# Kernel tuning notes

Measured on AMD Instinct MI355X. Metric: run time of the kernel, lower is better.

Reference implementation:

```python
import jax, jax.numpy as jnp
import numpy as np

N_NODES = 50000
VOCAB = 2048
HID = 256
N_EDGES = 1600000


def setup_inputs() -> dict:
    key = jax.random.key(0)
    ks = jax.random.split(key, 7)
    context = jax.random.normal(ks[0], (N_NODES, VOCAB), dtype=jnp.float32)
    adj_row = jax.random.randint(ks[1], (N_EDGES,), 0, N_NODES, dtype=jnp.int64)
    adj_col = jax.random.randint(ks[2], (N_EDGES,), 0, N_NODES, dtype=jnp.int64)
    adj_val = jax.random.uniform(ks[3], (N_EDGES,), dtype=jnp.float32)
    # learned params
    context_weight = jax.random.normal(ks[4], (HID, VOCAB), dtype=jnp.float32) * 0.02
    out_w = jax.random.normal(ks[5], (VOCAB, HID), dtype=jnp.float32) * 0.02
    out_b = jnp.zeros((VOCAB,), dtype=jnp.float32)
    return {
        "context": context,
        "adj_row": adj_row,
        "adj_col": adj_col,
        "adj_val": adj_val,
        "context_weight": context_weight,
        "out_w": out_w,
        "out_b": out_b,
    }


def reference(context, adj_row, adj_col, adj_val, context_weight, out_w, out_b):
    # support = context @ context_weight.T : [N, hid]
    support = jnp.einsum('nv,hv->nh', context, context_weight)
    # spmm: out[r] += val * support[c]  (COO sparse-dense matmul)
    gathered = support[adj_col] * adj_val[:, None]          # [E, hid]
    agg = jax.ops.segment_sum(gathered, adj_row, num_segments=N_NODES)  # [N, hid]
    score = jax.nn.relu(agg)
    # out linear: hid -> vocab
    output = jnp.einsum('nh,vh->nv', score, out_w) + out_b  # [N, vocab]
    return output
```

## Files before the change

kernel.cpp:

```cpp
#include <hip/hip_runtime.h>
#include <hip/hip_bf16.h>

#define N_NODES 50000
#define VOCAB   2048
#define HID     256
#define N_EDGES 1600000

typedef __attribute__((ext_vector_type(8))) __bf16 bf16x8;
typedef __attribute__((ext_vector_type(4))) __bf16 bf16x4;
typedef __attribute__((ext_vector_type(4))) float  f32x4;

__device__ __forceinline__ void gl_lds16(const void* g, void* l) {
    __builtin_amdgcn_global_load_lds(
        (const __attribute__((address_space(1))) void*)g,
        (__attribute__((address_space(3))) void*)l, 16, 0, 0);
}

#define ZERO_NB 49
__global__ __launch_bounds__(256) void phase1(
    const float* __restrict__ w, __bf16* __restrict__ wb, int n4,
    int* __restrict__ cnt, int ncnt)
{
    int bid = blockIdx.x;
    if (bid < ZERO_NB) {
        const int base = bid * 1024 + threadIdx.x * 4;
        if (base + 3 < ncnt)      *(int4*)&cnt[base] = make_int4(0, 0, 0, 0);
        else                      for (int i = 0; i < 4; ++i)
                                      if (base + i < ncnt) cnt[base + i] = 0;
        return;
    }
    const int t = (bid - ZERO_NB) * 256 + threadIdx.x;
    if (t < n4) {
        const float4 v = ((const float4*)w)[t];
        bf16x4 p = { (__bf16)v.x, (__bf16)v.y, (__bf16)v.z, (__bf16)v.w };
        ((bf16x4*)wb)[t] = p;
    }
}

#define HIST_NB 96
#define CVTW_NB 64
__global__ __launch_bounds__(256) void phase2(
    const float*  __restrict__ Af,
    const __bf16* __restrict__ Bb,
    __bf16*       __restrict__ Cb,
    int M,
    const int*    __restrict__ arow, int* __restrict__ cnt, int E,
    const float*  __restrict__ w2,   __bf16* __restrict__ w2b, int n4w)
{
    const int tid = threadIdx.x;
    int bid = blockIdx.x;

    if (bid < HIST_NB) {
        const int stride = HIST_NB * 256;
        for (int e4 = bid * 256 + tid; e4 < E / 4; e4 += stride) {
            const int4 r = ((const int4*)arow)[e4];
            atomicAdd(&cnt[r.x], 1); atomicAdd(&cnt[r.y], 1);
            atomicAdd(&cnt[r.z], 1); atomicAdd(&cnt[r.w], 1);
        }
        return;
    }
    bid -= HIST_NB;
    if (bid < CVTW_NB) {
        const int stride = CVTW_NB * 256;
        for (int t = bid * 256 + tid; t < n4w; t += stride) {
            const float4 v = ((const float4*)w2)[t];
            bf16x4 p = { (__bf16)v.x, (__bf16)v.y, (__bf16)v.z, (__bf16)v.w };
            ((bf16x4*)w2b)[t] = p;
        }
        return;
    }
    bid -= CVTW_NB;

    constexpr int K = 2048, N = 256, BM = 64, BK = 32, nkt = K / BK;
    __shared__ float  sAf[3][BM * BK];
    __shared__ __bf16 sB [3][N  * BK];

    const int lane = tid & 63;
    const int wn   = tid >> 6;
    const int half = lane >> 4;
    const int r16  = lane & 15;
    const int m0   = bid * BM;

    f32x4 acc[4][4] = {};

    auto stage = [&](int kt, int b) {
        const int k0 = kt * BK;
        #pragma unroll
        for (int i = 0; i < 2; ++i) {
            const int s   = i * 256 + tid;
            const int row = s >> 3, c = s & 7;
            const int csw = c ^ (row & 7);
            int gr = m0 + row; if (gr >= M) gr = M - 1;
            gl_lds16(&Af[(size_t)gr * K + k0 + csw * 4], &sAf[b][s * 4]);
        }
        #pragma unroll
        for (int i = 0; i < 4; ++i) {
            const int s   = i * 256 + tid;
            const int row = s >> 2, c = s & 3;
            const int csw = c ^ (row & 3);
            gl_lds16(&Bb[(size_t)row * K + k0 + csw * 8], &sB[b][s * 8]);
        }
    };
    auto step = [&](int b) {
        bf16x8 bfr[4];
        #pragma unroll
        for (int n = 0; n < 4; ++n) {
            const int brow = wn * 64 + n * 16 + r16;
            bfr[n] = *(const bf16x8*)&sB[b][brow * 32 + (half ^ (brow & 3)) * 8];
        }
        #pragma unroll
        for (int m = 0; m < 4; ++m) {
            const int arw = m * 16 + r16;
            const int rx  = arw & 7;
            const f32x4 lo = *(const f32x4*)&sAf[b][arw * 32 + ((2 * half)     ^ rx) * 4];
            const f32x4 hi = *(const f32x4*)&sAf[b][arw * 32 + ((2 * half + 1) ^ rx) * 4];
            const bf16x8 af = { (__bf16)lo.x, (__bf16)lo.y, (__bf16)lo.z, (__bf16)lo.w,
                                (__bf16)hi.x, (__bf16)hi.y, (__bf16)hi.z, (__bf16)hi.w };
            #pragma unroll
            for (int n = 0; n < 4; ++n)
                acc[m][n] = __builtin_amdgcn_mfma_f32_16x16x32_bf16(
                                af, bfr[n], acc[m][n], 0, 0, 0);
        }
    };

    stage(0, 0);
    stage(1, 1);
    for (int t = 0; t < nkt; ++t) {
        if (t + 1 < nkt) asm volatile("s_waitcnt vmcnt(6)" ::: "memory");
        else             asm volatile("s_waitcnt vmcnt(0)" ::: "memory");
        __builtin_amdgcn_s_barrier();
        __builtin_amdgcn_sched_barrier(0);
        step(t % 3);
        if (t + 2 < nkt) stage(t + 2, (t + 2) % 3);
    }

    #pragma unroll
    for (int m = 0; m < 4; ++m) {
        #pragma unroll
        for (int j = 0; j < 4; ++j) {
            const int gr = m0 + m * 16 + half * 4 + j;
            if (gr >= M) continue;
            #pragma unroll
            for (int n = 0; n < 4; ++n) {
                const int gc = wn * 64 + n * 16 + r16;
                Cb[(size_t)gr * N + gc] = (__bf16)acc[m][n][j];
            }
        }
    }
}

#define SCAN_NB 49

__global__ __launch_bounds__(256) void scan1(
    const int* __restrict__ cnt, int* __restrict__ bsum, int n)
{
    __shared__ int red[256];
    const int base = blockIdx.x * 1024 + threadIdx.x * 4;
    int s = 0;
    #pragma unroll
    for (int i = 0; i < 4; ++i) { const int idx = base + i; if (idx < n) s += cnt[idx]; }
    red[threadIdx.x] = s;
    __syncthreads();
    for (int off = 128; off > 0; off >>= 1) {
        if (threadIdx.x < off) red[threadIdx.x] += red[threadIdx.x + off];
        __syncthreads();
    }
    if (threadIdx.x == 0) bsum[blockIdx.x] = red[0];
}

__global__ __launch_bounds__(64) void scan2(int* __restrict__ bsum, int nb)
{
    if (threadIdx.x == 0) {
        int run = 0;
        for (int b = 0; b < nb; ++b) { const int v = bsum[b]; bsum[b] = run; run += v; }
        bsum[nb] = run;
    }
}

__global__ __launch_bounds__(256) void scan3(
    const int* __restrict__ cnt, const int* __restrict__ bsum,
    int* __restrict__ ptr, int* __restrict__ cursor, int n)
{
    __shared__ int hs[256];
    const int base = blockIdx.x * 1024 + threadIdx.x * 4;
    int loc[4]; int s = 0;
    #pragma unroll
    for (int i = 0; i < 4; ++i) {
        const int idx = base + i;
        loc[i] = (idx < n) ? cnt[idx] : 0;
        s += loc[i];
    }
    hs[threadIdx.x] = s;
    __syncthreads();
    for (int off = 1; off < 256; off <<= 1) {
        int v = (threadIdx.x >= off) ? hs[threadIdx.x - off] : 0;
        __syncthreads();
        hs[threadIdx.x] += v;
        __syncthreads();
    }
    int run = bsum[blockIdx.x] + ((threadIdx.x == 0) ? 0 : hs[threadIdx.x - 1]);
    #pragma unroll
    for (int i = 0; i < 4; ++i) {
        const int idx = base + i;
        if (idx < n) { ptr[idx] = run; cursor[idx] = run; }
        run += loc[i];
    }
    if (blockIdx.x == SCAN_NB - 1 && threadIdx.x == 255) ptr[n] = run;
}

__global__ __launch_bounds__(256) void csr_fill(
    const int*   __restrict__ arow,
    const int*   __restrict__ acol,
    const float* __restrict__ aval,
    int*         __restrict__ cursor,
    int2*        __restrict__ cpair,
    int E)
{
    const int stride = gridDim.x * blockDim.x;
    for (int e4 = blockIdx.x * blockDim.x + threadIdx.x; e4 < E / 4; e4 += stride) {
        const int4   r = ((const int4*)arow)[e4];
        const int4   c = ((const int4*)acol)[e4];
        const float4 v = ((const float4*)aval)[e4];
        int p;
        p = atomicAdd(&cursor[r.x], 1); cpair[p] = make_int2(c.x, __float_as_int(v.x));
        p = atomicAdd(&cursor[r.y], 1); cpair[p] = make_int2(c.y, __float_as_int(v.y));
        p = atomicAdd(&cursor[r.z], 1); cpair[p] = make_int2(c.z, __float_as_int(v.z));
        p = atomicAdd(&cursor[r.w], 1); cpair[p] = make_int2(c.w, __float_as_int(v.w));
    }
}

__global__ __launch_bounds__(256) void spmm_gather(
    const int*    __restrict__ ptr,
    const int2*   __restrict__ cpair,
    const __bf16* __restrict__ support,
    __bf16*       __restrict__ agg,
    int n)
{
    const int tid  = threadIdx.x;
    const int lane = tid & 63;
    const int row  = blockIdx.x * 4 + (tid >> 6);
    if (row >= n) return;
    const int l32 = lane & 31, ep = lane >> 5;
    const int beg = ptr[row], end = ptr[row + 1];

    float a[8] = {0.f, 0.f, 0.f, 0.f, 0.f, 0.f, 0.f, 0.f};

    auto fma8 = [&](float v, const uint4& s) {
        a[0] += v * __uint_as_float(s.x << 16);
        a[1] += v * __uint_as_float(s.x & 0xFFFF0000u);
        a[2] += v * __uint_as_float(s.y << 16);
        a[3] += v * __uint_as_float(s.y & 0xFFFF0000u);
        a[4] += v * __uint_as_float(s.z << 16);
        a[5] += v * __uint_as_float(s.z & 0xFFFF0000u);
        a[6] += v * __uint_as_float(s.w << 16);
        a[7] += v * __uint_as_float(s.w & 0xFFFF0000u);
    };

    int i = beg;
    for (; i + 8 <= end; i += 8) {
        const int2 p0 = cpair[i + ep];
        const int2 p1 = cpair[i + 2 + ep];
        const int2 p2 = cpair[i + 4 + ep];
        const int2 p3 = cpair[i + 6 + ep];
        const uint4 s0 = *(const uint4*)&support[(size_t)p0.x * HID + l32 * 8];
        const uint4 s1 = *(const uint4*)&support[(size_t)p1.x * HID + l32 * 8];
        const uint4 s2 = *(const uint4*)&support[(size_t)p2.x * HID + l32 * 8];
        const uint4 s3 = *(const uint4*)&support[(size_t)p3.x * HID + l32 * 8];
        fma8(__int_as_float(p0.y), s0);
        fma8(__int_as_float(p1.y), s1);
        fma8(__int_as_float(p2.y), s2);
        fma8(__int_as_float(p3.y), s3);
    }
    for (; i + 2 <= end; i += 2) {
        const int2 p = cpair[i + ep];
        const uint4 s = *(const uint4*)&support[(size_t)p.x * HID + l32 * 8];
        fma8(__int_as_float(p.y), s);
    }
    if (i < end && ep == 0) {
        const int2 p = cpair[i];
        const uint4 s = *(const uint4*)&support[(size_t)p.x * HID + l32 * 8];
        fma8(__int_as_float(p.y), s);
    }

    #pragma unroll
    for (int k = 0; k < 8; ++k) a[k] += __shfl_xor(a[k], 32);

    if (ep == 0) {
        bf16x8 o = { (__bf16)fmaxf(a[0], 0.f), (__bf16)fmaxf(a[1], 0.f),
                     (__bf16)fmaxf(a[2], 0.f), (__bf16)fmaxf(a[3], 0.f),
                     (__bf16)fmaxf(a[4], 0.f), (__bf16)fmaxf(a[5], 0.f),
                     (__bf16)fmaxf(a[6], 0.f), (__bf16)fmaxf(a[7], 0.f) };
        *(bf16x8*)&agg[(size_t)row * HID + l32 * 8] = o;
    }
}

__global__ __launch_bounds__(256) void gemm2(
    const __bf16* __restrict__ Ab,
    const __bf16* __restrict__ Bb,
    const float*  __restrict__ bias,
    float*        __restrict__ C,
    int M)
{
    constexpr int K = 256, N = 2048, BM = 128, BN = 128, BK = 32;
    constexpr int NBY = N / BN, nkt = K / BK;
    __shared__ __bf16 sA[3][BM * BK];
    __shared__ __bf16 sB[3][BN * BK];

    const int tid  = threadIdx.x;
    const int lane = tid & 63;
    const int wid  = tid >> 6;
    const int wm   = wid >> 1;
    const int wn   = wid & 1;
    const int half = lane >> 4;
    const int r16  = lane & 15;

    const int nwg = gridDim.x, cpx = nwg >> 3;
    const int wg  = (blockIdx.x & 7) * cpx + (blockIdx.x >> 3);
    const int m0  = (wg / NBY) * BM;
    const int n0  = (wg % NBY) * BN;

    f32x4 acc[4][4] = {};

    auto stage = [&](int kt, int b) {
        const int k0 = kt * BK;
        #pragma unroll
        for (int i = 0; i < 2; ++i) {
            const int s   = i * 256 + tid;
            const int row = s >> 2, c = s & 3;
            const int csw = c ^ (row & 3);
            int gr = m0 + row; if (gr >= M) gr = M - 1;
            gl_lds16(&Ab[(size_t)gr * K + k0 + csw * 8], &sA[b][s * 8]);
        }
        #pragma unroll
        for (int i = 0; i < 2; ++i) {
            const int s   = i * 256 + tid;
            const int row = s >> 2, c = s & 3;
            const int csw = c ^ (row & 3);
            gl_lds16(&Bb[(size_t)(n0 + row) * K + k0 + csw * 8], &sB[b][s * 8]);
        }
    };
    auto step = [&](int b) {
        bf16x8 bfr[4];
        #pragma unroll
        for (int n = 0; n < 4; ++n) {
            const int brow = wn * 64 + n * 16 + r16;
            bfr[n] = *(const bf16x8*)&sB[b][brow * 32 + (half ^ (brow & 3)) * 8];
        }
        #pragma unroll
        for (int m = 0; m < 4; ++m) {
            const int arw = wm * 64 + m * 16 + r16;
            const bf16x8 af = *(const bf16x8*)&sA[b][arw * 32 + (half ^ (arw & 3)) * 8];
            #pragma unroll
            for (int n = 0; n < 4; ++n)
                acc[m][n] = __builtin_amdgcn_mfma_f32_16x16x32_bf16(
                                af, bfr[n], acc[m][n], 0, 0, 0);
        }
    };

    stage(0, 0);
    stage(1, 1);
    for (int t = 0; t < nkt; ++t) {
        if (t + 1 < nkt) asm volatile("s_waitcnt vmcnt(4)" ::: "memory");
        else             asm volatile("s_waitcnt vmcnt(0)" ::: "memory");
        __builtin_amdgcn_s_barrier();
        __builtin_amdgcn_sched_barrier(0);
        step(t % 3);
        if (t + 2 < nkt) stage(t + 2, (t + 2) % 3);
    }

    #pragma unroll
    for (int m = 0; m < 4; ++m) {
        #pragma unroll
        for (int j = 0; j < 4; ++j) {
            const int gr = m0 + wm * 64 + m * 16 + half * 4 + j;
            if (gr >= M) continue;
            #pragma unroll
            for (int n = 0; n < 4; ++n) {
                const int gc = n0 + wn * 64 + n * 16 + r16;
                __builtin_nontemporal_store(acc[m][n][j] + bias[gc],
                                            &C[(size_t)gr * N + gc]);
            }
        }
    }
}

extern "C" void kernel_launch(void* const* d_in, const int* in_sizes, int n_in,
                              void* d_out, int out_size, void* d_ws, size_t ws_size,
                              hipStream_t stream) {
    const float* context  = (const float*)d_in[0];
    const int*   adj_row  = (const int*)  d_in[1];
    const int*   adj_col  = (const int*)  d_in[2];
    const float* adj_val  = (const float*)d_in[3];
    const float* ctx_w    = (const float*)d_in[4];
    const float* out_w    = (const float*)d_in[5];
    const float* out_b    = (const float*)d_in[6];
    float*       out      = (float*)d_out;

    char* ws = (char*)d_ws;
    __bf16* support_b = (__bf16*)ws;  ws += (size_t)N_NODES * HID * 2;
    __bf16* agg_b     = (__bf16*)ws;  ws += (size_t)N_NODES * HID * 2;
    __bf16* ctxw_b    = (__bf16*)ws;  ws += (size_t)HID * VOCAB * 2;
    __bf16* outw_b    = (__bf16*)ws;  ws += (size_t)VOCAB * HID * 2;
    int*    csr_ptr   = (int*)ws;     ws += ((size_t)N_NODES + 16) * 4;
    int*    cnt       = (int*)ws;     ws += (size_t)N_NODES * 4;
    int*    cursor    = (int*)ws;     ws += (size_t)N_NODES * 4;
    int*    bsum      = (int*)ws;     ws += ((size_t)SCAN_NB + 16) * 4;
    int2*   cpair     = (int2*)ws;    ws += (size_t)N_EDGES * 8;

    constexpr int N4 = HID * VOCAB / 4;

    phase1<<<dim3(ZERO_NB + (N4 + 255) / 256), 256, 0, stream>>>(
        ctx_w, ctxw_b, N4, cnt, N_NODES);

    phase2<<<dim3(HIST_NB + CVTW_NB + (N_NODES + 63) / 64), 256, 0, stream>>>(
        context, ctxw_b, support_b, N_NODES,
        adj_row, cnt, N_EDGES,
        out_w, outw_b, N4);

    scan1<<<SCAN_NB, 256, 0, stream>>>(cnt, bsum, N_NODES);
    scan2<<<1, 64, 0, stream>>>(bsum, SCAN_NB);
    scan3<<<SCAN_NB, 256, 0, stream>>>(cnt, bsum, csr_ptr, cursor, N_NODES);

    csr_fill<<<512, 256, 0, stream>>>(
        adj_row, adj_col, adj_val, cursor, cpair, N_EDGES);

    spmm_gather<<<(N_NODES + 3) / 4, 256, 0, stream>>>(
        csr_ptr, cpair, support_b, agg_b, N_NODES);

    gemm2<<<dim3(((N_NODES + 127) / 128) * (VOCAB / 128)), 256, 0, stream>>>(
        agg_b, outw_b, out_b, out, N_NODES);
}
```

Before: 491.9 us.

## Regroup launches: fuse CSR fill with first GEMM, load B operand directly

Moves the context GEMM out of the histogram kernel and into the CSR fill kernel, so the fill's atomic scatter overlaps the dense matmul. Histogram and both weight conversions now share one launch, and a memset zeroes the counts. Both GEMMs stop staging the weight operand in LDS and read B fragments straight from global memory, with A double-buffered and synced by __syncthreads. This cuts LDS traffic and frees capacity, but exposes global latency on B loads and replaces the hand-tuned vmcnt pipeline with full barriers.

```diff
diff --git a/kernel.cpp b/kernel.cpp
--- a/kernel.cpp
+++ b/kernel.cpp
@@ -16,40 +16,15 @@
         (__attribute__((address_space(3))) void*)l, 16, 0, 0);
 }
 
-#define ZERO_NB 49
+#define HIST_NB 256
+#define CVT_NB  512
 __global__ __launch_bounds__(256) void phase1(
-    const float* __restrict__ w, __bf16* __restrict__ wb, int n4,
-    int* __restrict__ cnt, int ncnt)
-{
-    int bid = blockIdx.x;
-    if (bid < ZERO_NB) {
-        const int base = bid * 1024 + threadIdx.x * 4;
-        if (base + 3 < ncnt)      *(int4*)&cnt[base] = make_int4(0, 0, 0, 0);
-        else                      for (int i = 0; i < 4; ++i)
-                                      if (base + i < ncnt) cnt[base + i] = 0;
-        return;
-    }
-    const int t = (bid - ZERO_NB) * 256 + threadIdx.x;
-    if (t < n4) {
-        const float4 v = ((const float4*)w)[t];
-        bf16x4 p = { (__bf16)v.x, (__bf16)v.y, (__bf16)v.z, (__bf16)v.w };
-        ((bf16x4*)wb)[t] = p;
-    }
-}
-
-#define HIST_NB 96
-#define CVTW_NB 64
-__global__ __launch_bounds__(256) void phase2(
-    const float*  __restrict__ Af,
-    const __bf16* __restrict__ Bb,
-    __bf16*       __restrict__ Cb,
-    int M,
-    const int*    __restrict__ arow, int* __restrict__ cnt, int E,
-    const float*  __restrict__ w2,   __bf16* __restrict__ w2b, int n4w)
+    const int*   __restrict__ arow, int* __restrict__ cnt, int E,
+    const float* __restrict__ w1, __bf16* __restrict__ w1b,
+    const float* __restrict__ w2, __bf16* __restrict__ w2b)
 {
     const int tid = threadIdx.x;
     int bid = blockIdx.x;
-
     if (bid < HIST_NB) {
         const int stride = HIST_NB * 256;
         for (int e4 = bid * 256 + tid; e4 < E / 4; e4 += stride) {
@@ -60,20 +35,108 @@
         return;
     }
     bid -= HIST_NB;
-    if (bid < CVTW_NB) {
-        const int stride = CVTW_NB * 256;
-        for (int t = bid * 256 + tid; t < n4w; t += stride) {
-            const float4 v = ((const float4*)w2)[t];
-            bf16x4 p = { (__bf16)v.x, (__bf16)v.y, (__bf16)v.z, (__bf16)v.w };
-            ((bf16x4*)w2b)[t] = p;
+    const float* w  = (bid < CVT_NB) ? w1 : w2;
+    __bf16*      wb = (bid < CVT_NB) ? w1b : w2b;
+    if (bid >= CVT_NB) bid -= CVT_NB;
+    const int t = bid * 256 + tid;
+    const float4 v = ((const float4*)w)[t];
+    bf16x4 p = { (__bf16)v.x, (__bf16)v.y, (__bf16)v.z, (__bf16)v.w };
+    ((bf16x4*)wb)[t] = p;
+}
+
+#define SCAN_NB 49
+
+__global__ __launch_bounds__(256) void scan1(
+    const int* __restrict__ cnt, int* __restrict__ bsum, int n)
+{
+    __shared__ int red[256];
+    const int base = blockIdx.x * 1024 + threadIdx.x * 4;
+    int s = 0;
+    #pragma unroll
+    for (int i = 0; i < 4; ++i) { const int idx = base + i; if (idx < n) s += cnt[idx]; }
+    red[threadIdx.x] = s;
+    __syncthreads();
+    for (int off = 128; off > 0; off >>= 1) {
+        if (threadIdx.x < off) red[threadIdx.x] += red[threadIdx.x + off];
+        __syncthreads();
+    }
+    if (threadIdx.x == 0) bsum[blockIdx.x] = red[0];
+}
+
+__global__ __launch_bounds__(64) void scan2(int* __restrict__ bsum, int nb)
+{
+    if (threadIdx.x == 0) {
+        int run = 0;
+        for (int b = 0; b < nb; ++b) { const int v = bsum[b]; bsum[b] = run; run += v; }
+        bsum[nb] = run;
+    }
+}
+
+__global__ __launch_bounds__(256) void scan3(
+    const int* __restrict__ cnt, const int* __restrict__ bsum,
+    int* __restrict__ ptr, int* __restrict__ cursor, int n)
+{
+    __shared__ int hs[256];
+    const int base = blockIdx.x * 1024 + threadIdx.x * 4;
+    int loc[4]; int s = 0;
+    #pragma unroll
+    for (int i = 0; i < 4; ++i) {
+        const int idx = base + i;
+        loc[i] = (idx < n) ? cnt[idx] : 0;
+        s += loc[i];
+    }
+    hs[threadIdx.x] = s;
+    __syncthreads();
+    for (int off = 1; off < 256; off <<= 1) {
+        int v = (threadIdx.x >= off) ? hs[threadIdx.x - off] : 0;
+        __syncthreads();
+        hs[threadIdx.x] += v;
+        __syncthreads();
+    }
+    int run = bsum[blockIdx.x] + ((threadIdx.x == 0) ? 0 : hs[threadIdx.x - 1]);
+    #pragma unroll
+    for (int i = 0; i < 4; ++i) {
+        const int idx = base + i;
+        if (idx < n) { ptr[idx] = run; cursor[idx] = run; }
+        run += loc[i];
+    }
+    if (blockIdx.x == SCAN_NB - 1 && threadIdx.x == 255) ptr[n] = run;
+}
+
+#define FILL_NB 256
+__global__ __launch_bounds__(256) void fill_gemm1(
+    const int*    __restrict__ arow,
+    const int*    __restrict__ acol,
+    const float*  __restrict__ aval,
+    int*          __restrict__ cursor,
+    int2*         __restrict__ cpair,
+    int E,
+    const float*  __restrict__ Af,
+    const __bf16* __restrict__ Bb,
+    __bf16*       __restrict__ Cb,
+    int M)
+{
+    const int tid = threadIdx.x;
+    int bid = blockIdx.x;
+
+    if (bid < FILL_NB) {
+        const int stride = FILL_NB * 256;
+        for (int e4 = bid * 256 + tid; e4 < E / 4; e4 += stride) {
+            const int4   r = ((const int4*)arow)[e4];
+            const int4   c = ((const int4*)acol)[e4];
+            const float4 v = ((const float4*)aval)[e4];
+            int p;
+            p = atomicAdd(&cursor[r.x], 1); cpair[p] = make_int2(c.x, __float_as_int(v.x));
+            p = atomicAdd(&cursor[r.y], 1); cpair[p] = make_int2(c.y, __float_as_int(v.y));
+            p = atomicAdd(&cursor[r.z], 1); cpair[p] = make_int2(c.z, __float_as_int(v.z));
+            p = atomicAdd(&cursor[r.w], 1); cpair[p] = make_int2(c.w, __float_as_int(v.w));
         }
         return;
     }
-    bid -= CVTW_NB;
+    bid -= FILL_NB;
 
     constexpr int K = 2048, N = 256, BM = 64, BK = 32, nkt = K / BK;
-    __shared__ float  sAf[3][BM * BK];
-    __shared__ __bf16 sB [3][N  * BK];
+    __shared__ float sAf[2][BM * BK];
 
     const int lane = tid & 63;
     const int wn   = tid >> 6;
@@ -83,7 +146,7 @@
 
     f32x4 acc[4][4] = {};
 
-    auto stage = [&](int kt, int b) {
+    auto stageA = [&](int kt, int b) {
         const int k0 = kt * BK;
         #pragma unroll
         for (int i = 0; i < 2; ++i) {
@@ -93,21 +156,19 @@
             int gr = m0 + row; if (gr >= M) gr = M - 1;
             gl_lds16(&Af[(size_t)gr * K + k0 + csw * 4], &sAf[b][s * 4]);
         }
-        #pragma unroll
-        for (int i = 0; i < 4; ++i) {
-            const int s   = i * 256 + tid;
-            const int row = s >> 2, c = s & 3;
-            const int csw = c ^ (row & 3);
-            gl_lds16(&Bb[(size_t)row * K + k0 + csw * 8], &sB[b][s * 8]);
-        }
     };
-    auto step = [&](int b) {
-        bf16x8 bfr[4];
+
+    stageA(0, 0);
+    __syncthreads();
+    for (int t = 0; t < nkt; ++t) {
+        uint4 bq[4];
         #pragma unroll
         for (int n = 0; n < 4; ++n) {
             const int brow = wn * 64 + n * 16 + r16;
-            bfr[n] = *(const bf16x8*)&sB[b][brow * 32 + (half ^ (brow & 3)) * 8];
-        }
+            bq[n] = *(const uint4*)&Bb[(size_t)brow * K + t * BK + half * 8];
+        }
+        if (t + 1 < nkt) stageA(t + 1, (t + 1) & 1);
+        const int b = t & 1;
         #pragma unroll
         for (int m = 0; m < 4; ++m) {
             const int arw = m * 16 + r16;
@@ -119,19 +180,9 @@
             #pragma unroll
             for (int n = 0; n < 4; ++n)
                 acc[m][n] = __builtin_amdgcn_mfma_f32_16x16x32_bf16(
-                                af, bfr[n], acc[m][n], 0, 0, 0);
-        }
-    };
-
-    stage(0, 0);
-    stage(1, 1);
-    for (int t = 0; t < nkt; ++t) {
-        if (t + 1 < nkt) asm volatile("s_waitcnt vmcnt(6)" ::: "memory");
-        else             asm volatile("s_waitcnt vmcnt(0)" ::: "memory");
-        __builtin_amdgcn_s_barrier();
-        __builtin_amdgcn_sched_barrier(0);
-        step(t % 3);
-        if (t + 2 < nkt) stage(t + 2, (t + 2) % 3);
+                                af, *(const bf16x8*)&bq[n], acc[m][n], 0, 0, 0);
+        }
+        __syncthreads();
     }
 
     #pragma unroll
@@ -146,86 +197,6 @@
                 Cb[(size_t)gr * N + gc] = (__bf16)acc[m][n][j];
             }
         }
-    }
-}
-
-#define SCAN_NB 49
-
-__global__ __launch_bounds__(256) void scan1(
-    const int* __restrict__ cnt, int* __restrict__ bsum, int n)
-{
-    __shared__ int red[256];
-    const int base = blockIdx.x * 1024 + threadIdx.x * 4;
-    int s = 0;
-    #pragma unroll
-    for (int i = 0; i < 4; ++i) { const int idx = base + i; if (idx < n) s += cnt[idx]; }
-    red[threadIdx.x] = s;
-    __syncthreads();
-    for (int off = 128; off > 0; off >>= 1) {
-        if (threadIdx.x < off) red[threadIdx.x] += red[threadIdx.x + off];
-        __syncthreads();
-    }
-    if (threadIdx.x == 0) bsum[blockIdx.x] = red[0];
-}
-
-__global__ __launch_bounds__(64) void scan2(int* __restrict__ bsum, int nb)
-{
-    if (threadIdx.x == 0) {
-        int run = 0;
-        for (int b = 0; b < nb; ++b) { const int v = bsum[b]; bsum[b] = run; run += v; }
-        bsum[nb] = run;
-    }
-}
-
-__global__ __launch_bounds__(256) void scan3(
-    const int* __restrict__ cnt, const int* __restrict__ bsum,
-    int* __restrict__ ptr, int* __restrict__ cursor, int n)
-{
-    __shared__ int hs[256];
-    const int base = blockIdx.x * 1024 + threadIdx.x * 4;
-    int loc[4]; int s = 0;
-    #pragma unroll
-    for (int i = 0; i < 4; ++i) {
-        const int idx = base + i;
-        loc[i] = (idx < n) ? cnt[idx] : 0;
-        s += loc[i];
-    }
-    hs[threadIdx.x] = s;
-    __syncthreads();
-    for (int off = 1; off < 256; off <<= 1) {
-        int v = (threadIdx.x >= off) ? hs[threadIdx.x - off] : 0;
-        __syncthreads();
-        hs[threadIdx.x] += v;
-        __syncthreads();
-    }
-    int run = bsum[blockIdx.x] + ((threadIdx.x == 0) ? 0 : hs[threadIdx.x - 1]);
-    #pragma unroll
-    for (int i = 0; i < 4; ++i) {
-        const int idx = base + i;
-        if (idx < n) { ptr[idx] = run; cursor[idx] = run; }
-        run += loc[i];
-    }
-    if (blockIdx.x == SCAN_NB - 1 && threadIdx.x == 255) ptr[n] = run;
-}
-
-__global__ __launch_bounds__(256) void csr_fill(
-    const int*   __restrict__ arow,
-    const int*   __restrict__ acol,
-    const float* __restrict__ aval,
-    int*         __restrict__ cursor,
-    int2*        __restrict__ cpair,
-    int E)
-{
-    const int stride = gridDim.x * blockDim.x;
-    for (int e4 = blockIdx.x * blockDim.x + threadIdx.x; e4 < E / 4; e4 += stride) {
-        const int4   r = ((const int4*)arow)[e4];
-        const int4   c = ((const int4*)acol)[e4];
-        const float4 v = ((const float4*)aval)[e4];
-        int p;
-        p = atomicAdd(&cursor[r.x], 1); cpair[p] = make_int2(c.x, __float_as_int(v.x));
-        p = atomicAdd(&cursor[r.y], 1); cpair[p] = make_int2(c.y, __float_as_int(v.y));
-        p = atomicAdd(&cursor[r.z], 1); cpair[p] = make_int2(c.z, __float_as_int(v.z));
-        p = atomicAdd(&cursor[r.w], 1); cpair[p] = make_int2(c.w, __float_as_int(v.w));
     }
 }
 
@@ -303,8 +274,7 @@
 {
     constexpr int K = 256, N = 2048, BM = 128, BN = 128, BK = 32;
     constexpr int NBY = N / BN, nkt = K / BK;
-    __shared__ __bf16 sA[3][BM * BK];
-    __shared__ __bf16 sB[3][BN * BK];
+    __shared__ __bf16 sA[2][BM * BK];
 
     const int tid  = threadIdx.x;
     const int lane = tid & 63;
@@ -321,7 +291,7 @@
 
     f32x4 acc[4][4] = {};
 
-    auto stage = [&](int kt, int b) {
+    auto stageA = [&](int kt, int b) {
         const int k0 = kt * BK;
         #pragma unroll
         for (int i = 0; i < 2; ++i) {
@@ -331,21 +301,19 @@
             int gr = m0 + row; if (gr >= M) gr = M - 1;
             gl_lds16(&Ab[(size_t)gr * K + k0 + csw * 8], &sA[b][s * 8]);
         }
-        #pragma unroll
-        for (int i = 0; i < 2; ++i) {
-            const int s   = i * 256 + tid;
-            const int row = s >> 2, c = s & 3;
-            const int csw = c ^ (row & 3);
-            gl_lds16(&Bb[(size_t)(n0 + row) * K + k0 + csw * 8], &sB[b][s * 8]);
-        }
     };
-    auto step = [&](int b) {
-        bf16x8 bfr[4];
+
+    stageA(0, 0);
+    __syncthreads();
+    for (int t = 0; t < nkt; ++t) {
+        uint4 bq[4];
         #pragma unroll
         for (int n = 0; n < 4; ++n) {
-            const int brow = wn * 64 + n * 16 + r16;
-            bfr[n] = *(const bf16x8*)&sB[b][brow * 32 + (half ^ (brow & 3)) * 8];
-        }
+            const int brow = n0 + wn * 64 + n * 16 + r16;
+            bq[n] = *(const uint4*)&Bb[(size_t)brow * K + t * BK + half * 8];
+        }
+        if (t + 1 < nkt) stageA(t + 1, (t + 1) & 1);
+        const int b = t & 1;
         #pragma unroll
         for (int m = 0; m < 4; ++m) {
             const int arw = wm * 64 + m * 16 + r16;
@@ -353,19 +321,9 @@
             #pragma unroll
             for (int n = 0; n < 4; ++n)
                 acc[m][n] = __builtin_amdgcn_mfma_f32_16x16x32_bf16(
-                                af, bfr[n], acc[m][n], 0, 0, 0);
-        }
-    };
-
-    stage(0, 0);
-    stage(1, 1);
-    for (int t = 0; t < nkt; ++t) {
-        if (t + 1 < nkt) asm volatile("s_waitcnt vmcnt(4)" ::: "memory");
-        else             asm volatile("s_waitcnt vmcnt(0)" ::: "memory");
-        __builtin_amdgcn_s_barrier();
-        __builtin_amdgcn_sched_barrier(0);
-        step(t % 3);
-        if (t + 2 < nkt) stage(t + 2, (t + 2) % 3);
+                                af, *(const bf16x8*)&bq[n], acc[m][n], 0, 0, 0);
+        }
+        __syncthreads();
     }
 
     #pragma unroll
@@ -407,22 +365,18 @@
     int*    bsum      = (int*)ws;     ws += ((size_t)SCAN_NB + 16) * 4;
     int2*   cpair     = (int2*)ws;    ws += (size_t)N_EDGES * 8;
 
-    constexpr int N4 = HID * VOCAB / 4;
-
-    phase1<<<dim3(ZERO_NB + (N4 + 255) / 256), 256, 0, stream>>>(
-        ctx_w, ctxw_b, N4, cnt, N_NODES);
-
-    phase2<<<dim3(HIST_NB + CVTW_NB + (N_NODES + 63) / 64), 256, 0, stream>>>(
-        context, ctxw_b, support_b, N_NODES,
-        adj_row, cnt, N_EDGES,
-        out_w, outw_b, N4);
+    hipMemsetAsync(cnt, 0, (size_t)N_NODES * 4, stream);
+
+    phase1<<<dim3(HIST_NB + 2 * CVT_NB), 256, 0, stream>>>(
+        adj_row, cnt, N_EDGES, ctx_w, ctxw_b, out_w, outw_b);
 
     scan1<<<SCAN_NB, 256, 0, stream>>>(cnt, bsum, N_NODES);
     scan2<<<1, 64, 0, stream>>>(bsum, SCAN_NB);
     scan3<<<SCAN_NB, 256, 0, stream>>>(cnt, bsum, csr_ptr, cursor, N_NODES);
 
-    csr_fill<<<512, 256, 0, stream>>>(
-        adj_row, adj_col, adj_val, cursor, cpair, N_EDGES);
+    fill_gemm1<<<dim3(FILL_NB + (N_NODES + 63) / 64), 256, 0, stream>>>(
+        adj_row, adj_col, adj_val, cursor, cpair, N_EDGES,
+        context, ctxw_b, support_b, N_NODES);
 
     spmm_gather<<<(N_NODES + 3) / 4, 256, 0, stream>>>(
         csr_ptr, cpair, support_b, agg_b, N_NODES);
```

New measurement: 581.9 us. 18.3% more time.

## Fuse block-prefix scan into final scan kernel and deepen SpMM gather unroll

Applied to the files above, without the earlier changes.

Removes the single-threaded scan2 kernel. Each scan3m block now reduces the preceding block sums itself in shared memory, which saves one kernel launch and a serial pass. The final pointer is set directly to the edge count. Separately, the SpMM gather loop now handles 16 edges per iteration with 8 independent support loads in flight to raise memory-level parallelism, at the cost of more registers and a longer remainder path for short rows.

```diff
diff --git a/kernel.cpp b/kernel.cpp
--- a/kernel.cpp
+++ b/kernel.cpp
@@ -168,21 +168,22 @@
     if (threadIdx.x == 0) bsum[blockIdx.x] = red[0];
 }
 
-__global__ __launch_bounds__(64) void scan2(int* __restrict__ bsum, int nb)
-{
-    if (threadIdx.x == 0) {
-        int run = 0;
-        for (int b = 0; b < nb; ++b) { const int v = bsum[b]; bsum[b] = run; run += v; }
-        bsum[nb] = run;
-    }
-}
-
-__global__ __launch_bounds__(256) void scan3(
+__global__ __launch_bounds__(256) void scan3m(
     const int* __restrict__ cnt, const int* __restrict__ bsum,
-    int* __restrict__ ptr, int* __restrict__ cursor, int n)
+    int* __restrict__ ptr, int* __restrict__ cursor, int n, int E)
 {
     __shared__ int hs[256];
-    const int base = blockIdx.x * 1024 + threadIdx.x * 4;
+    __shared__ int pre[256];
+    const int tid = threadIdx.x;
+    pre[tid] = (tid < blockIdx.x && tid < SCAN_NB) ? bsum[tid] : 0;
+    __syncthreads();
+    for (int off = 128; off > 0; off >>= 1) {
+        if (tid < off) pre[tid] += pre[tid + off];
+        __syncthreads();
+    }
+    const int bbase = pre[0];
+
+    const int base = blockIdx.x * 1024 + tid * 4;
     int loc[4]; int s = 0;
     #pragma unroll
     for (int i = 0; i < 4; ++i) {
@@ -190,22 +191,22 @@
         loc[i] = (idx < n) ? cnt[idx] : 0;
         s += loc[i];
     }
-    hs[threadIdx.x] = s;
+    hs[tid] = s;
     __syncthreads();
     for (int off = 1; off < 256; off <<= 1) {
-        int v = (threadIdx.x >= off) ? hs[threadIdx.x - off] : 0;
+        int v = (tid >= off) ? hs[tid - off] : 0;
         __syncthreads();
-        hs[threadIdx.x] += v;
+        hs[tid] += v;
         __syncthreads();
     }
-    int run = bsum[blockIdx.x] + ((threadIdx.x == 0) ? 0 : hs[threadIdx.x - 1]);
+    int run = bbase + ((tid == 0) ? 0 : hs[tid - 1]);
     #pragma unroll
     for (int i = 0; i < 4; ++i) {
         const int idx = base + i;
         if (idx < n) { ptr[idx] = run; cursor[idx] = run; }
         run += loc[i];
     }
-    if (blockIdx.x == SCAN_NB - 1 && threadIdx.x == 255) ptr[n] = run;
+    if (blockIdx.x == 0 && tid == 0) ptr[n] = E;
 }
 
 __global__ __launch_bounds__(256) void csr_fill(
@@ -257,19 +258,16 @@
     };
 
     int i = beg;
-    for (; i + 8 <= end; i += 8) {
-        const int2 p0 = cpair[i + ep];
-        const int2 p1 = cpair[i + 2 + ep];
-        const int2 p2 = cpair[i + 4 + ep];
-        const int2 p3 = cpair[i + 6 + ep];
-        const uint4 s0 = *(const uint4*)&support[(size_t)p0.x * HID + l32 * 8];
-        const uint4 s1 = *(const uint4*)&support[(size_t)p1.x * HID + l32 * 8];
-        const uint4 s2 = *(const uint4*)&support[(size_t)p2.x * HID + l32 * 8];
-        const uint4 s3 = *(const uint4*)&support[(size_t)p3.x * HID + l32 * 8];
-        fma8(__int_as_float(p0.y), s0);
-        fma8(__int_as_float(p1.y), s1);
-        fma8(__int_as_float(p2.y), s2);
-        fma8(__int_as_float(p3.y), s3);
+    for (; i + 16 <= end; i += 16) {
+        int2 p[8];
+        #pragma unroll
+        for (int u = 0; u < 8; ++u) p[u] = cpair[i + 2 * u + ep];
+        uint4 s[8];
+        #pragma unroll
+        for (int u = 0; u < 8; ++u)
+            s[u] = *(const uint4*)&support[(size_t)p[u].x * HID + l32 * 8];
+        #pragma unroll
+        for (int u = 0; u < 8; ++u) fma8(__int_as_float(p[u].y), s[u]);
     }
     for (; i + 2 <= end; i += 2) {
         const int2 p = cpair[i + ep];
@@ -404,7 +402,7 @@
     int*    csr_ptr   = (int*)ws;     ws += ((size_t)N_NODES + 16) * 4;
     int*    cnt       = (int*)ws;     ws += (size_t)N_NODES * 4;
     int*    cursor    = (int*)ws;     ws += (size_t)N_NODES * 4;
-    int*    bsum      = (int*)ws;     ws += ((size_t)SCAN_NB + 16) * 4;
+    int*    bsum      = (int*)ws;     ws += 320;
     int2*   cpair     = (int2*)ws;    ws += (size_t)N_EDGES * 8;
 
     constexpr int N4 = HID * VOCAB / 4;
@@ -418,8 +416,7 @@
         out_w, outw_b, N4);
 
     scan1<<<SCAN_NB, 256, 0, stream>>>(cnt, bsum, N_NODES);
-    scan2<<<1, 64, 0, stream>>>(bsum, SCAN_NB);
-    scan3<<<SCAN_NB, 256, 0, stream>>>(cnt, bsum, csr_ptr, cursor, N_NODES);
+    scan3m<<<SCAN_NB, 256, 0, stream>>>(cnt, bsum, csr_ptr, cursor, N_NODES, N_EDGES);
 
     csr_fill<<<512, 256, 0, stream>>>(
         adj_row, adj_col, adj_val, cursor, cpair, N_EDGES);
```

Result: no change. 494.1 us (+0.4%).
